# Kernel optimization log

Hardware: AMD Instinct MI355X
Metric: run time of the kernel (lower is better)

## Reference

```python
import jax, jax.numpy as jnp
import numpy as np
from jax import lax

GRAVITY = 9.8
DT = 0.1
MAX_STEPS = 200


def _conv(x, w, b):
    # x: [N,C,H,W], w: [O,I,3,3] (PyTorch OIHW), padding=1 -> SAME
    y = lax.conv_general_dilated(x, w, window_strides=(1, 1), padding='SAME',
                                 dimension_numbers=('NCHW', 'OIHW', 'NCHW'))
    return y + b[None, :, None, None]


def _maxpool2(x):
    return lax.reduce_window(x, -jnp.inf, lax.max,
                             window_dimensions=(1, 1, 2, 2),
                             window_strides=(1, 1, 2, 2), padding='VALID')


def setup_inputs() -> dict:
    key = jax.random.key(0)
    ks = jax.random.split(key, 12)
    B = 256
    x = jax.random.normal(ks[0], (B, 12, 128, 128), dtype=jnp.float32)

    def he(k, shape, fan_in):
        return jax.random.normal(k, shape, dtype=jnp.float32) * np.float32(np.sqrt(2.0 / fan_in))

    w1 = he(ks[1], (32, 12, 3, 3), 12 * 9); b1 = jnp.zeros((32,), jnp.float32)
    w2 = he(ks[2], (64, 32, 3, 3), 32 * 9); b2 = jnp.zeros((64,), jnp.float32)
    w3 = he(ks[3], (64, 64, 3, 3), 64 * 9); b3 = jnp.zeros((64,), jnp.float32)
    w4 = he(ks[4], (64, 64, 3, 3), 64 * 9); b4 = jnp.zeros((64,), jnp.float32)
    wl1 = he(ks[5], (128, 64 * 8 * 8), 64 * 8 * 8); bl1 = jnp.zeros((128,), jnp.float32)
    wl2 = he(ks[6], (4, 128), 128); bl2 = jnp.zeros((4,), jnp.float32)
    return {'x': x, 'w1': w1, 'b1': b1, 'w2': w2, 'b2': b2, 'w3': w3, 'b3': b3,
            'w4': w4, 'b4': b4, 'wl1': wl1, 'bl1': bl1, 'wl2': wl2, 'bl2': bl2}


def _forward(x, w1, b1, w2, b2, w3, b3, w4, b4, wl1, bl1, wl2, bl2):
    h = _maxpool2(jax.nn.relu(_conv(x, w1, b1)))   # [B,32,64,64]
    h = _maxpool2(jax.nn.relu(_conv(h, w2, b2)))   # [B,64,32,32]
    h = _maxpool2(jax.nn.relu(_conv(h, w3, b3)))   # [B,64,16,16]
    h = _maxpool2(jax.nn.relu(_conv(h, w4, b4)))   # [B,64,8,8]
    h = h.reshape(h.shape[0], -1)                  # [B,4096]
    h = jax.nn.relu(h @ wl1.T + bl1)               # [B,128]
    state = h @ wl2.T + bl2                        # [B,4]

    px, py, vx, vy = state[:, 0], state[:, 1], state[:, 2], state[:, 3]

    def step(carry, _):
        cx, cy, cvy = carry
        nvy = cvy - GRAVITY * DT
        nx = cx + vx * DT
        ny = jnp.maximum(cy + nvy * DT, 0.0)
        return (nx, ny, nvy), None

    (fx, _, _), _ = lax.scan(step, (px, py, vy), None, length=MAX_STEPS)
    return fx


def reference(x, w1, b1, w2, b2, w3, b3, w4, b4, wl1, bl1, wl2, bl2):
    return _forward(x, w1, b1, w2, b2, w3, b3, w4, b4, wl1, bl1, wl2, bl2)
```

## Files before the change

### kernel.cpp

```cpp
#include <hip/hip_runtime.h>


typedef _Float16 f16;
typedef _Float16 f16x8 __attribute__((ext_vector_type(8)));
typedef _Float16 f16x4 __attribute__((ext_vector_type(4)));
typedef float f32x4 __attribute__((ext_vector_type(4)));
typedef float f32x16 __attribute__((ext_vector_type(16)));

__global__ __launch_bounds__(512)
void pack_all(const float* __restrict__ w1, const float* __restrict__ w2,
              const float* __restrict__ w3, const float* __restrict__ w4,
              const float* __restrict__ wl1, f16* __restrict__ apack,
              f16* __restrict__ wl1h) {
  if (blockIdx.x >= 189) {
    int i = ((blockIdx.x - 189) * 512 + threadIdx.x) * 4;
    float4 v = *(const float4*)(wl1 + i);
    f16x4 h = { (f16)v.x, (f16)v.y, (f16)v.z, (f16)v.w };
    *(f16x4*)(wl1h + i) = h;
    return;
  }
  int idx = blockIdx.x * 512 + threadIdx.x;
  int frag = idx >> 9;
  int e = idx & 511;
  int lane = e >> 3, j = e & 7;
  float v = 0.f;
  if (frag < 9) {
    int kh = frag / 3, kw = frag % 3;
    int oc = lane & 31;
    int ic = (lane >> 5) * 8 + j;
    if (ic < 12) v = w1[((oc * 12 + ic) * 3 + kh) * 3 + kw];
  } else if (frag < 45) {
    int f = frag - 9;
    int ocg = f & 1;
    int sk = f >> 1;
    int ks = sk & 1, sh = sk >> 1;
    int kh = sh / 3, kw = sh % 3;
    int oc = ocg * 32 + (lane & 31);
    int ic = ks * 16 + (lane >> 5) * 8 + j;
    v = w2[((oc * 32 + ic) * 3 + kh) * 3 + kw];
  } else if (frag < 117) {
    int f = frag - 45;
    int ocg = f & 1;
    int sk = f >> 1;
    int ks = sk & 3, sh = sk >> 2;
    int kh = sh / 3, kw = sh % 3;
    int oc = ocg * 32 + (lane & 31);
    int ic = ks * 16 + (lane >> 5) * 8 + j;
    v = w3[((oc * 64 + ic) * 3 + kh) * 3 + kw];
  } else {
    int f = frag - 117;
    int sk = f >> 2, og = f & 3;
    int sh = sk >> 1, ks = sk & 1;
    int kh = sh / 3, kw = sh % 3;
    int row16 = lane & 15, kg = lane >> 4;
    int oc = og * 16 + row16;
    int ic = ks * 32 + kg * 8 + j;
    v = w4[((oc * 64 + ic) * 3 + kh) * 3 + kw];
  }
  apack[idx] = (f16)v;
}

__global__ __launch_bounds__(512)
void conv1_mfma(const float* __restrict__ x, const f16* __restrict__ apack,
                const float* __restrict__ bias, f16* __restrict__ hout) {
  constexpr int W = 128, H = 128;
  constexpr int PADB = 48, ROWB = 130 * PADB;
  constexpr int TPB = 8;
  __shared__ char smem[6 * ROWB];
  const int tid = threadIdx.x;
  const int n = blockIdx.y;
  const int R0 = blockIdx.x * (TPB * 4);

  if (tid < 36) {
    int slot = tid / 6, r = tid % 6;
    int px = (r >= 3) ? 129 : 0;
    int ch = r % 3;
    *(float4*)(smem + slot * ROWB + px * PADB + ch * 16) =
        make_float4(0.f, 0.f, 0.f, 0.f);
  }

  const int g = tid >> 4;
  const int l16 = tid & 15;
  const int Q = l16 >> 2, q = l16 & 3;

  auto load_row = [&](int ri) -> float4 {
    float4 v = make_float4(0.f, 0.f, 0.f, 0.f);
    if (l16 < 12 && ri >= 0 && ri < H)
      v = *(const float4*)(x + ((size_t)(n * 12 + l16) * H + ri) * W + g * 4);
    return v;
  };
  auto xpose_write = [&](float4 av, int slot) {
    float4 t1, t2;
    {
      float sx = __shfl_xor(av.x, 1), sy = __shfl_xor(av.y, 1);
      float sz = __shfl_xor(av.z, 1), sw = __shfl_xor(av.w, 1);
      bool odd = q & 1;
      t1.x = odd ? sy : av.x;  t1.y = odd ? av.y : sx;
      t1.z = odd ? sw : av.z;  t1.w = odd ? av.w : sz;
    }
    {
      float sx = __shfl_xor(t1.x, 2), sy = __shfl_xor(t1.y, 2);
      float sz = __shfl_xor(t1.z, 2), sw = __shfl_xor(t1.w, 2);
      bool hi2 = q & 2;
      t2.x = hi2 ? sz : t1.x;  t2.y = hi2 ? sw : t1.y;
      t2.z = hi2 ? t1.z : sx;  t2.w = hi2 ? t1.w : sy;
    }
    f16x4 h = { (f16)t2.x, (f16)t2.y, (f16)t2.z, (f16)t2.w };
    *(f16x4*)(smem + slot * ROWB + (g * 4 + q + 1) * PADB + Q * 8) = h;
  };

  const int wv = tid >> 6, l = tid & 63;
  const int rp = wv >> 2;
  const int pxb = (wv & 3) * 32;
  const int rl0 = rp * 2;
  const int ln = l & 31;
  const int hi = l >> 5;

  f16x8 A[9];
#pragma unroll
  for (int ks = 0; ks < 9; ++ks)
    A[ks] = *(const f16x8*)(apack + ((ks << 9) + (l << 3)));

  float4 a[6];
#pragma unroll
  for (int i = 0; i < 6; ++i) a[i] = load_row(R0 - 1 + i);
#pragma unroll
  for (int i = 0; i < 6; ++i) xpose_write(a[i], i);
  __syncthreads();

  int s0 = 0;
  for (int t = 0; t < TPB; ++t) {
    if (t + 1 < TPB) {
#pragma unroll
      for (int i = 0; i < 4; ++i) a[i] = load_row(R0 + 4 * t + 5 + i);
    }
    f32x16 acc0 = (f32x16)0.f, acc1 = (f32x16)0.f;
#pragma unroll
    for (int kw = 0; kw < 3; ++kw) {
      const char* bcol = smem + (pxb + ln + kw) * PADB + hi * 16;
      f16x8 R[4];
#pragma unroll
      for (int j = 0; j < 4; ++j) {
        int sl = s0 + rl0 + j; if (sl >= 6) sl -= 6;
        R[j] = *(const f16x8*)(bcol + sl * ROWB);
      }
#pragma unroll
      for (int kh = 0; kh < 3; ++kh) {
        acc0 = __builtin_amdgcn_mfma_f32_32x32x16_f16(A[kh * 3 + kw], R[kh],     acc0, 0, 0, 0);
        acc1 = __builtin_amdgcn_mfma_f32_32x32x16_f16(A[kh * 3 + kw], R[kh + 1], acc1, 0, 0, 0);
      }
    }
    {
      const int pr = (R0 >> 1) + 2 * t + rp;
#pragma unroll
      for (int gg = 0; gg < 4; ++gg) {
        float v[4];
#pragma unroll
        for (int c = 0; c < 4; ++c) {
          float m = fmaxf(acc0[gg * 4 + c], acc1[gg * 4 + c]);
          v[c] = fmaxf(m, __shfl_xor(m, 1));
        }
        if ((l & 1) == 0) {
          const int pw = (pxb + ln) >> 1;
          const int oc0 = gg * 8 + hi * 4;
          f16x4 pk;
#pragma unroll
          for (int c = 0; c < 4; ++c)
            pk[c] = (f16)fmaxf(v[c] + bias[oc0 + c], 0.f);
          *(f16x4*)(hout + (((size_t)(n * 64 + pr) * 64 + pw) * 32 + oc0)) = pk;
        }
      }
    }
    __syncthreads();
    if (t + 1 < TPB) {
#pragma unroll
      for (int i = 0; i < 4; ++i) {
        int sl = s0 + i; if (sl >= 6) sl -= 6;
        xpose_write(a[i], sl);
      }
      __syncthreads();
    }
    s0 += 4; if (s0 >= 6) s0 -= 6;
  }
}

__global__ __launch_bounds__(256)
void conv2_roll(const f16* __restrict__ hin, const f16* __restrict__ apack,
                const float* __restrict__ bias, f16* __restrict__ hout) {
  constexpr int C = 32, W = 64, H = 64;
  constexpr int PADB = 80, ROWB = 66 * PADB;
  constexpr int TPB = 4;
  __shared__ char smem[6 * ROWB];
  const int tid = threadIdx.x;
  const int n = blockIdx.y;
  const int R0 = blockIdx.x * (TPB * 4);

  auto chunk_ld = [&](int c, int rbase) -> float4 {
    int rowl = c / 264, rem = c - rowl * 264;
    int px = rem >> 2, kc = rem & 3;
    int ri = rbase + rowl, gx = px - 1;
    float4 v = make_float4(0.f, 0.f, 0.f, 0.f);
    if (ri >= 0 && ri < H && gx >= 0 && gx < W)
      v = *(const float4*)(hin + (((size_t)(n * H + ri) * W + gx) * C + kc * 8));
    return v;
  };
  auto chunk_st = [&](int c, int sbase, float4 v) {
    int rowl = c / 264, rem = c - rowl * 264;
    int px = rem >> 2, kc = rem & 3;
    int slot = sbase + rowl; if (slot >= 6) slot -= 6;
    *(float4*)(smem + slot * ROWB + px * PADB + kc * 16) = v;
  };

  {
    float4 a[7];
#pragma unroll
    for (int it = 0; it < 7; ++it) {
      int c = tid + it * 256;
      a[it] = (c < 1584) ? chunk_ld(c, R0 - 1) : make_float4(0.f, 0.f, 0.f, 0.f);
    }
#pragma unroll
    for (int it = 0; it < 7; ++it) {
      int c = tid + it * 256;
      if (c < 1584) chunk_st(c, 0, a[it]);
    }
  }
  __syncthreads();

  const int wv = tid >> 6, l = tid & 63;
  const int rp = wv >> 1;
  const int pxb = (wv & 1) * 32;
  const int rl0 = rp * 2;
  const int ln = l & 31;
  const int hi = l >> 5;

  float4 a[5];
  int s04 = 0;
  for (int t = 0; t < TPB; ++t) {
    if (t + 1 < TPB) {
#pragma unroll
      for (int it = 0; it < 5; ++it) {
        int c = tid + it * 256;
        a[it] = (c < 1056) ? chunk_ld(c, R0 + 4 * t + 5)
                           : make_float4(0.f, 0.f, 0.f, 0.f);
      }
    }
    f32x16 acc[2][2];
    acc[0][0] = (f32x16)0.f; acc[0][1] = (f32x16)0.f;
    acc[1][0] = (f32x16)0.f; acc[1][1] = (f32x16)0.f;
#pragma unroll
    for (int sh = 0; sh < 9; ++sh) {
      const int kh = sh / 3, kw = sh % 3;
      f16x8 A[2][2];
#pragma unroll
      for (int ks = 0; ks < 2; ++ks)
#pragma unroll
        for (int ocg = 0; ocg < 2; ++ocg)
          A[ks][ocg] = *(const f16x8*)(apack + ((((sh * 2 + ks) * 2 + ocg) << 9) + (l << 3)));
#pragma unroll
      for (int rowi = 0; rowi < 2; ++rowi) {
        int sl = s04 + rl0 + rowi + kh; if (sl >= 6) sl -= 6;
        const char* base = smem + sl * ROWB + (pxb + ln + kw) * PADB + hi * 16;
#pragma unroll
        for (int ks = 0; ks < 2; ++ks) {
          f16x8 B = *(const f16x8*)(base + ks * 32);
          acc[rowi][0] = __builtin_amdgcn_mfma_f32_32x32x16_f16(A[ks][0], B, acc[rowi][0], 0, 0, 0);
          acc[rowi][1] = __builtin_amdgcn_mfma_f32_32x32x16_f16(A[ks][1], B, acc[rowi][1], 0, 0, 0);
        }
      }
    }
    {
      const int pr = (R0 >> 1) + 2 * t + rp;
#pragma unroll
      for (int ocg = 0; ocg < 2; ++ocg) {
#pragma unroll
        for (int gg = 0; gg < 4; ++gg) {
          float v[4];
#pragma unroll
          for (int c = 0; c < 4; ++c) {
            float m = fmaxf(acc[0][ocg][gg * 4 + c], acc[1][ocg][gg * 4 + c]);
            v[c] = fmaxf(m, __shfl_xor(m, 1));
          }
          if ((l & 1) == 0) {
            const int pw = (pxb + ln) >> 1;
            const int oc0 = ocg * 32 + gg * 8 + hi * 4;
            f16x4 pk;
#pragma unroll
            for (int c = 0; c < 4; ++c)
              pk[c] = (f16)fmaxf(v[c] + bias[oc0 + c], 0.f);
            *(f16x4*)(hout + (((size_t)(n * 32 + pr) * 32 + pw) * 64 + oc0)) = pk;
          }
        }
      }
    }
    __syncthreads();
    if (t + 1 < TPB) {
#pragma unroll
      for (int it = 0; it < 5; ++it) {
        int c = tid + it * 256;
        if (c < 1056) chunk_st(c, s04, a[it]);
      }
      __syncthreads();
    }
    s04 += 4; if (s04 >= 6) s04 -= 6;
  }
}

template<int C, int W, int H, int BR, int PADB>
__global__ __launch_bounds__(256)
void conv_shift32(const f16* __restrict__ hin, const f16* __restrict__ apack,
                  const float* __restrict__ bias, f16* __restrict__ hout) {
  constexpr int KS16 = C / 16;
  constexpr int SR = BR + 2;
  constexpr int ROWB = (W + 2) * PADB;
  __shared__ char smem[SR * ROWB];
  const int tid = threadIdx.x;
  const int n = blockIdx.y;
  const int r0 = blockIdx.x * BR;
  constexpr int CPC = C / 8;
  constexpr int TOTC = SR * (W + 2) * CPC;
  constexpr int NITER = (TOTC + 255) / 256;
  {
    float4 stg[NITER];
#pragma unroll
    for (int it = 0; it < NITER; ++it) {
      const int t = tid + it * 256;
      float4 v = make_float4(0.f, 0.f, 0.f, 0.f);
      if (t < TOTC) {
        int sr = t / ((W + 2) * CPC);
        int rem = t - sr * ((W + 2) * CPC);
        int px = rem / CPC;
        int kc = rem - px * CPC;
        int ri = r0 + sr - 1;
        int gx = px - 1;
        if (ri >= 0 && ri < H && gx >= 0 && gx < W)
          v = *(const float4*)(hin + (((size_t)(n * H + ri) * W + gx) * C + kc * 8));
      }
      stg[it] = v;
    }
#pragma unroll
    for (int it = 0; it < NITER; ++it) {
      const int t = tid + it * 256;
      if (t < TOTC) {
        int sr = t / ((W + 2) * CPC);
        int rem = t - sr * ((W + 2) * CPC);
        int px = rem / CPC;
        int kc = rem - px * CPC;
        *(float4*)(smem + sr * ROWB + px * PADB + kc * 16) = stg[it];
      }
    }
  }
  __syncthreads();

  const int wv = tid >> 6, l = tid & 63;
  constexpr int WPP = W / 32;
  const int rp = wv / WPP;
  const int pxb = (wv % WPP) * 32;
  const int rl0 = rp * 2;
  const int ln = l & 31;
  const int hi = l >> 5;
  const int px0 = pxb + ln;

  f32x16 acc[2][2];
  acc[0][0] = (f32x16)0.f; acc[0][1] = (f32x16)0.f;
  acc[1][0] = (f32x16)0.f; acc[1][1] = (f32x16)0.f;

#pragma unroll
  for (int sh = 0; sh < 9; ++sh) {
    const int kh = sh / 3, kw = sh % 3;
    f16x8 A[KS16][2];
#pragma unroll
    for (int ks = 0; ks < KS16; ++ks)
#pragma unroll
      for (int ocg = 0; ocg < 2; ++ocg)
        A[ks][ocg] = *(const f16x8*)(apack + ((((sh * KS16 + ks) * 2 + ocg) << 9) + (l << 3)));
#pragma unroll
    for (int rowi = 0; rowi < 2; ++rowi) {
      const char* base = smem + (rl0 + rowi + kh) * ROWB + (px0 + kw) * PADB + hi * 16;
#pragma unroll
      for (int ks = 0; ks < KS16; ++ks) {
        f16x8 B = *(const f16x8*)(base + ks * 32);
        acc[rowi][0] = __builtin_amdgcn_mfma_f32_32x32x16_f16(A[ks][0], B, acc[rowi][0], 0, 0, 0);
        acc[rowi][1] = __builtin_amdgcn_mfma_f32_32x32x16_f16(A[ks][1], B, acc[rowi][1], 0, 0, 0);
      }
    }
  }
  constexpr int PH = H / 2, PW = W / 2;
  const int pr = blockIdx.x * (BR / 2) + rp;
#pragma unroll
  for (int ocg = 0; ocg < 2; ++ocg) {
#pragma unroll
    for (int gg = 0; gg < 4; ++gg) {
      float v[4];
#pragma unroll
      for (int c = 0; c < 4; ++c) {
        float m = fmaxf(acc[0][ocg][gg * 4 + c], acc[1][ocg][gg * 4 + c]);
        v[c] = fmaxf(m, __shfl_xor(m, 1));
      }
      if ((l & 1) == 0) {
        const int pw = (pxb + ln) >> 1;
        const int oc0 = ocg * 32 + gg * 8 + hi * 4;
        f16x4 pk;
#pragma unroll
        for (int c = 0; c < 4; ++c)
          pk[c] = (f16)fmaxf(v[c] + bias[oc0 + c], 0.f);
        *(f16x4*)(hout + (((size_t)(n * PH + pr) * PW + pw) * 64 + oc0)) = pk;
      }
    }
  }
}

__global__ __launch_bounds__(512)
void tail_fused(const f16* __restrict__ hin, const f16* __restrict__ apack4,
                const float* __restrict__ bias, const f16* __restrict__ wl1h,
                const float* __restrict__ bl1, const float* __restrict__ wl2,
                const float* __restrict__ bl2, float* __restrict__ out) {
  constexpr int C = 64, W = 16, H = 16;
  constexpr int PADB = 144, ROWB = 18 * PADB;
  __shared__ char smem[18 * ROWB];
  __shared__ float hbuf[4096];
  __shared__ float red[4 * 128];
  __shared__ float red2[128];
  const int tid = threadIdx.x;
  const int n = blockIdx.x;

  constexpr int CPC = 8, TOTC = 18 * 18 * CPC;
  {
    float4 stg[6];
#pragma unroll
    for (int it = 0; it < 6; ++it) {
      const int t = tid + it * 512;
      float4 v = make_float4(0.f, 0.f, 0.f, 0.f);
      if (t < TOTC) {
        int sr = t / (18 * CPC);
        int rem = t - sr * (18 * CPC);
        int px = rem / CPC;
        int kc = rem - px * CPC;
        int ri = sr - 1, gx = px - 1;
        if (ri >= 0 && ri < H && gx >= 0 && gx < W)
          v = *(const float4*)(hin + (((size_t)(n * H + ri) * W + gx) * C + kc * 8));
      }
      stg[it] = v;
    }
#pragma unroll
    for (int it = 0; it < 6; ++it) {
      const int t = tid + it * 512;
      if (t < TOTC) {
        int sr = t / (18 * CPC);
        int rem = t - sr * (18 * CPC);
        int px = rem / CPC;
        int kc = rem - px * CPC;
        *(float4*)(smem + sr * ROWB + px * PADB + kc * 16) = stg[it];
      }
    }
  }
  __syncthreads();

  {
    const int wv = tid >> 6, l = tid & 63;
    const int lp = l & 15, kg = l >> 4;
    const int rl0 = wv * 2;

    f32x4 acc[2][4];
#pragma unroll
    for (int a = 0; a < 2; ++a)
#pragma unroll
      for (int o = 0; o < 4; ++o) acc[a][o] = (f32x4){0.f, 0.f, 0.f, 0.f};

#pragma unroll
    for (int sh = 0; sh < 9; ++sh) {
      const int kh = sh / 3, kw = sh % 3;
      f16x8 A[2][4];
#pragma unroll
      for (int ks = 0; ks < 2; ++ks)
#pragma unroll
        for (int og = 0; og < 4; ++og)
          A[ks][og] = *(const f16x8*)(apack4 + ((((sh * 2 + ks) * 4 + og) << 9) + (l << 3)));
#pragma unroll
      for (int rowi = 0; rowi < 2; ++rowi) {
        const char* base = smem + (rl0 + rowi + kh) * ROWB;
#pragma unroll
        for (int ks = 0; ks < 2; ++ks) {
          f16x8 B = *(const f16x8*)(base + (lp + kw) * PADB + ks * 64 + kg * 16);
#pragma unroll
          for (int og = 0; og < 4; ++og)
            acc[rowi][og] =
                __builtin_amdgcn_mfma_f32_16x16x32_f16(A[ks][og], B, acc[rowi][og], 0, 0, 0);
        }
      }
    }
#pragma unroll
    for (int og = 0; og < 4; ++og) {
      float v[4];
#pragma unroll
      for (int c = 0; c < 4; ++c) {
        float m = fmaxf(acc[0][og][c], acc[1][og][c]);
        v[c] = fmaxf(m, __shfl_xor(m, 1));
      }
      if ((l & 1) == 0) {
        const int pw = lp >> 1;
        const int oc0 = og * 16 + kg * 4;
#pragma unroll
        for (int c = 0; c < 4; ++c)
          hbuf[(oc0 + c) * 64 + wv * 8 + pw] = fmaxf(v[c] + bias[oc0 + c], 0.f);
      }
    }
  }
  __syncthreads();

  {
    const int nn = tid & 127;
    const int ks = tid >> 7;
    const f16x8* wp = (const f16x8*)(wl1h + (size_t)nn * 4096 + ks * 1024);
    const float4* xr = (const float4*)(&hbuf[ks * 1024]);
    float s = 0.f;
#pragma unroll 4
    for (int i = 0; i < 128; ++i) {
      f16x8 w8 = wp[i];
      float4 a0 = xr[2 * i], a1 = xr[2 * i + 1];
      s = fmaf((float)w8[0], a0.x, fmaf((float)w8[1], a0.y,
          fmaf((float)w8[2], a0.z, fmaf((float)w8[3], a0.w, s))));
      s = fmaf((float)w8[4], a1.x, fmaf((float)w8[5], a1.y,
          fmaf((float)w8[6], a1.z, fmaf((float)w8[7], a1.w, s))));
    }
    red[ks * 128 + nn] = s;
  }
  __syncthreads();
  if (tid < 128) {
    float h = bl1[tid] + red[tid] + red[128 + tid] + red[256 + tid] + red[384 + tid];
    h = fmaxf(h, 0.f);
    red2[tid] = h * (wl2[tid] + 20.0f * wl2[256 + tid]);
  }
  __syncthreads();
#pragma unroll
  for (int s = 64; s > 0; s >>= 1) {
    if (tid < s) red2[tid] += red2[tid + s];
    __syncthreads();
  }
  if (tid == 0) out[n] = red2[0] + bl2[0] + 20.0f * bl2[2];
}

extern "C" void kernel_launch(void* const* d_in, const int* in_sizes, int n_in,
                              void* d_out, int out_size, void* d_ws, size_t ws_size,
                              hipStream_t stream) {
  const float* x   = (const float*)d_in[0];
  const float* w1  = (const float*)d_in[1];
  const float* b1  = (const float*)d_in[2];
  const float* w2  = (const float*)d_in[3];
  const float* b2  = (const float*)d_in[4];
  const float* w3  = (const float*)d_in[5];
  const float* b3  = (const float*)d_in[6];
  const float* w4  = (const float*)d_in[7];
  const float* b4  = (const float*)d_in[8];
  const float* wl1 = (const float*)d_in[9];
  const float* bl1 = (const float*)d_in[10];
  const float* wl2 = (const float*)d_in[11];
  const float* bl2 = (const float*)d_in[12];
  float* out = (float*)d_out;
  char* ws = (char*)d_ws;

  f16* apack = (f16*)ws;
  f16* wl1h  = (f16*)(ws + 524288u);
  f16* h1 = (f16*)(ws + 2097152u);
  f16* h2 = (f16*)(ws + 69206016u);
  f16* h3 = (f16*)(ws + 102760448u);

  pack_all<<<445, 512, 0, stream>>>(w1, w2, w3, w4, wl1, apack, wl1h);
  conv1_mfma<<<dim3(4, 256), 512, 0, stream>>>(x, apack, b1, h1);
  conv2_roll<<<dim3(4, 256), 256, 0, stream>>>(h1, apack + 9 * 512, b2, h2);
  conv_shift32<64, 32, 32, 8, 144><<<dim3(4, 256), 256, 0, stream>>>(
      h2, apack + 45 * 512, b3, h3);
  tail_fused<<<256, 512, 0, stream>>>(h3, apack + 117 * 512, b4, wl1h,
                                      bl1, wl2, bl2, out);
}
```

Measured before the change: 219.4 us.

## Replace LDS-staged conv1 with direct global-load conv per wave

Rewrites the first convolution to gather input pixels straight from global memory into MFMA operands, dropping the shared-memory row ring, shuffle transpose and block barriers. Blocks shrink to 256 threads with more blocks per image, each handling 4 pooled rows. This removes synchronisation and LDS traffic but re-reads overlapping input rows and columns from cache with scalar strided loads.

New measurement: 684.2 us. 212% more time.

```diff
diff --git a/kernel.cpp b/kernel.cpp
--- a/kernel.cpp
+++ b/kernel.cpp
@@ -60,89 +60,50 @@
   apack[idx] = (f16)v;
 }
 
-__global__ __launch_bounds__(512)
-void conv1_mfma(const float* __restrict__ x, const f16* __restrict__ apack,
-                const float* __restrict__ bias, f16* __restrict__ hout) {
-  constexpr int W = 128, H = 128;
-  constexpr int PADB = 48, ROWB = 130 * PADB;
-  constexpr int TPB = 8;
-  __shared__ char smem[6 * ROWB];
+__global__ __launch_bounds__(256, 3)
+void conv1_direct(const float* __restrict__ x, const f16* __restrict__ apack,
+                  const float* __restrict__ bias, f16* __restrict__ hout) {
+  constexpr int W = 128, H = 128, HW = W * H;
+  constexpr int TPW = 4;
+  const int n = blockIdx.y;
   const int tid = threadIdx.x;
-  const int n = blockIdx.y;
-  const int R0 = blockIdx.x * (TPB * 4);
-
-  if (tid < 36) {
-    int slot = tid / 6, r = tid % 6;
-    int px = (r >= 3) ? 129 : 0;
-    int ch = r % 3;
-    *(float4*)(smem + slot * ROWB + px * PADB + ch * 16) =
-        make_float4(0.f, 0.f, 0.f, 0.f);
-  }
-
-  const int g = tid >> 4;
-  const int l16 = tid & 15;
-  const int Q = l16 >> 2, q = l16 & 3;
-
-  auto load_row = [&](int ri) -> float4 {
-    float4 v = make_float4(0.f, 0.f, 0.f, 0.f);
-    if (l16 < 12 && ri >= 0 && ri < H)
-      v = *(const float4*)(x + ((size_t)(n * 12 + l16) * H + ri) * W + g * 4);
-    return v;
-  };
-  auto xpose_write = [&](float4 av, int slot) {
-    float4 t1, t2;
-    {
-      float sx = __shfl_xor(av.x, 1), sy = __shfl_xor(av.y, 1);
-      float sz = __shfl_xor(av.z, 1), sw = __shfl_xor(av.w, 1);
-      bool odd = q & 1;
-      t1.x = odd ? sy : av.x;  t1.y = odd ? av.y : sx;
-      t1.z = odd ? sw : av.z;  t1.w = odd ? av.w : sz;
-    }
-    {
-      float sx = __shfl_xor(t1.x, 2), sy = __shfl_xor(t1.y, 2);
-      float sz = __shfl_xor(t1.z, 2), sw = __shfl_xor(t1.w, 2);
-      bool hi2 = q & 2;
-      t2.x = hi2 ? sz : t1.x;  t2.y = hi2 ? sw : t1.y;
-      t2.z = hi2 ? t1.z : sx;  t2.w = hi2 ? t1.w : sy;
-    }
-    f16x4 h = { (f16)t2.x, (f16)t2.y, (f16)t2.z, (f16)t2.w };
-    *(f16x4*)(smem + slot * ROWB + (g * 4 + q + 1) * PADB + Q * 8) = h;
-  };
-
   const int wv = tid >> 6, l = tid & 63;
-  const int rp = wv >> 2;
-  const int pxb = (wv & 3) * 32;
-  const int rl0 = rp * 2;
+  const int pxb = wv * 32;
   const int ln = l & 31;
   const int hi = l >> 5;
+  const int pr0 = blockIdx.x * TPW;
 
   f16x8 A[9];
 #pragma unroll
   for (int ks = 0; ks < 9; ++ks)
     A[ks] = *(const f16x8*)(apack + ((ks << 9) + (l << 3)));
 
-  float4 a[6];
-#pragma unroll
-  for (int i = 0; i < 6; ++i) a[i] = load_row(R0 - 1 + i);
-#pragma unroll
-  for (int i = 0; i < 6; ++i) xpose_write(a[i], i);
-  __syncthreads();
-
-  int s0 = 0;
-  for (int t = 0; t < TPB; ++t) {
-    if (t + 1 < TPB) {
-#pragma unroll
-      for (int i = 0; i < 4; ++i) a[i] = load_row(R0 + 4 * t + 5 + i);
-    }
+  const float* xn = x + (size_t)n * 12 * HW + (size_t)(hi * 8) * HW;
+
+  for (int t = 0; t < TPW; ++t) {
+    const int pr = pr0 + t;
+    const int r0 = pr * 2 - 1;
     f32x16 acc0 = (f32x16)0.f, acc1 = (f32x16)0.f;
 #pragma unroll
     for (int kw = 0; kw < 3; ++kw) {
-      const char* bcol = smem + (pxb + ln + kw) * PADB + hi * 16;
+      const int pxc = pxb + ln + kw - 1;
+      const bool okc = (pxc >= 0 && pxc < W);
       f16x8 R[4];
 #pragma unroll
       for (int j = 0; j < 4; ++j) {
-        int sl = s0 + rl0 + j; if (sl >= 6) sl -= 6;
-        R[j] = *(const f16x8*)(bcol + sl * ROWB);
+        const int ri = r0 + j;
+        const bool okr = okc && (ri >= 0) && (ri < H);
+        const float* base = xn + (size_t)(okr ? ri : 0) * W + (okr ? pxc : 0);
+        float v[8];
+#pragma unroll
+        for (int jj = 0; jj < 8; ++jj) {
+          const bool ok = okr && (hi * 8 + jj < 12);
+          v[jj] = ok ? base[(size_t)jj * HW] : 0.f;
+        }
+        f16x8 b;
+#pragma unroll
+        for (int jj = 0; jj < 8; ++jj) b[jj] = (f16)v[jj];
+        R[j] = b;
       }
 #pragma unroll
       for (int kh = 0; kh < 3; ++kh) {
@@ -150,37 +111,24 @@
         acc1 = __builtin_amdgcn_mfma_f32_32x32x16_f16(A[kh * 3 + kw], R[kh + 1], acc1, 0, 0, 0);
       }
     }
-    {
-      const int pr = (R0 >> 1) + 2 * t + rp;
-#pragma unroll
-      for (int gg = 0; gg < 4; ++gg) {
-        float v[4];
-#pragma unroll
-        for (int c = 0; c < 4; ++c) {
-          float m = fmaxf(acc0[gg * 4 + c], acc1[gg * 4 + c]);
-          v[c] = fmaxf(m, __shfl_xor(m, 1));
-        }
-        if ((l & 1) == 0) {
-          const int pw = (pxb + ln) >> 1;
-          const int oc0 = gg * 8 + hi * 4;
-          f16x4 pk;
-#pragma unroll
-          for (int c = 0; c < 4; ++c)
-            pk[c] = (f16)fmaxf(v[c] + bias[oc0 + c], 0.f);
-          *(f16x4*)(hout + (((size_t)(n * 64 + pr) * 64 + pw) * 32 + oc0)) = pk;
-        }
-      }
-    }
-    __syncthreads();
-    if (t + 1 < TPB) {
-#pragma unroll
-      for (int i = 0; i < 4; ++i) {
-        int sl = s0 + i; if (sl >= 6) sl -= 6;
-        xpose_write(a[i], sl);
-      }
-      __syncthreads();
-    }
-    s0 += 4; if (s0 >= 6) s0 -= 6;
+#pragma unroll
+    for (int gg = 0; gg < 4; ++gg) {
+      float v[4];
+#pragma unroll
+      for (int c = 0; c < 4; ++c) {
+        float m = fmaxf(acc0[gg * 4 + c], acc1[gg * 4 + c]);
+        v[c] = fmaxf(m, __shfl_xor(m, 1));
+      }
+      if ((l & 1) == 0) {
+        const int pw = (pxb + ln) >> 1;
+        const int oc0 = gg * 8 + hi * 4;
+        f16x4 pk;
+#pragma unroll
+        for (int c = 0; c < 4; ++c)
+          pk[c] = (f16)fmaxf(v[c] + bias[oc0 + c], 0.f);
+        *(f16x4*)(hout + (((size_t)(n * 64 + pr) * 64 + pw) * 32 + oc0)) = pk;
+      }
+    }
   }
 }
 
@@ -565,7 +513,7 @@
   f16* h3 = (f16*)(ws + 102760448u);
 
   pack_all<<<445, 512, 0, stream>>>(w1, w2, w3, w4, wl1, apack, wl1h);
-  conv1_mfma<<<dim3(4, 256), 512, 0, stream>>>(x, apack, b1, h1);
+  conv1_direct<<<dim3(16, 256), 256, 0, stream>>>(x, apack, b1, h1);
   conv2_roll<<<dim3(4, 256), 256, 0, stream>>>(h1, apack + 9 * 512, b2, h2);
   conv_shift32<64, 32, 32, 8, 144><<<dim3(4, 256), 256, 0, stream>>>(
       h2, apack + 45 * 512, b3, h3);
```
